# Performance work log

Measured on AMD Instinct MI355X. Metric: run time of the kernel, lower is better.

Reference implementation:

```python
import jax, jax.numpy as jnp
import numpy as np
from jax import lax

NFFT, WIN, HOP = 512, 320, 160
PAD = NFFT // 2
F = NFFT // 2 + 1  # 257

def _window():
    # torch.hann_window(320, periodic=True), center-padded to n_fft=512 (torch.stft convention)
    w = 0.5 - 0.5 * jnp.cos(2.0 * jnp.pi * jnp.arange(WIN, dtype=jnp.float32) / WIN)
    lp = (NFFT - WIN) // 2
    return jnp.pad(w, (lp, NFFT - WIN - lp))

def _stft(x):  # [N, L] -> [N, T, F] complex64 (center=True, reflect pad)
    xp = jnp.pad(x, ((0, 0), (PAD, PAD)), mode='reflect')
    T = 1 + (xp.shape[1] - NFFT) // HOP
    idx = jnp.arange(T)[:, None] * HOP + jnp.arange(NFFT)[None, :]
    frames = xp[:, idx] * _window()  # [N, T, NFFT]
    return jnp.fft.rfft(frames, axis=-1)

def _istft(spec, length):  # [N, T, F] complex -> [N, length]
    win = _window()
    frames = jnp.fft.irfft(spec, n=NFFT, axis=-1) * win  # [N, T, NFFT]
    N, T, _ = frames.shape
    total = (T - 1) * HOP + NFFT
    pos = (jnp.arange(T)[:, None] * HOP + jnp.arange(NFFT)[None, :]).reshape(-1)
    out = jnp.zeros((N, total), frames.dtype).at[:, pos].add(frames.reshape(N, -1))
    wsq = jnp.zeros((total,), win.dtype).at[pos].add(jnp.tile(win * win, T))
    out = out / jnp.maximum(wsq, 1e-11)[None, :]
    return out[:, PAD:PAD + length]

def _lstm(x, W_ih, W_hh, b_ih, b_hh):  # x [N, T, D] -> [N, T, H]
    N, T, _ = x.shape
    H = W_hh.shape[1]
    xW = x @ W_ih.T + (b_ih + b_hh)  # precompute input projections [N, T, 4H]
    def step(carry, xt):
        h, c = carry
        g = xt + h @ W_hh.T
        i, f, gg, o = jnp.split(g, 4, axis=-1)  # torch gate order i,f,g,o
        c = jax.nn.sigmoid(f) * c + jax.nn.sigmoid(i) * jnp.tanh(gg)
        h = jax.nn.sigmoid(o) * jnp.tanh(c)
        return (h, c), h
    h0 = jnp.zeros((N, H), x.dtype)
    _, hs = lax.scan(step, (h0, h0), jnp.swapaxes(xW, 0, 1))
    return jnp.swapaxes(hs, 0, 1)

def _forward(x, W_ih, W_hh, b_ih, b_hh, W1, b1, W2, b2):
    B, L, C = x.shape
    xm = jnp.transpose(x, (0, 2, 1)).reshape(B * C, L)
    spec = _stft(xm).reshape(B, C, -1, F)  # [B, C, T, F] == r_spec + 1j*i_spec
    T = spec.shape[2]
    feat = jnp.concatenate([spec.real, spec.imag], axis=-1).reshape(B * C, T, 2 * F)
    h = _lstm(feat, W_ih, W_hh, b_ih, b_hh)  # [B*C, T, 128]
    def masked(Wl, bl):
        m = h @ Wl.T + bl                      # [B*C, T, 514]
        rm, im = jnp.split(m, 2, axis=-1)
        mask = (rm + 1j * im).reshape(B, C, T, F)
        return mask * spec                      # complex mask multiply
    s_spec = masked(W1, b1)
    n_spec = masked(W2, b2)
    # per-frequency PSD matrices over time
    psd_s = jnp.einsum('bctf,betf->bfce', s_spec, jnp.conj(s_spec)) / T
    psd_n = jnp.einsum('bctf,betf->bfce', n_spec, jnp.conj(n_spec)) / T
    tr_n = jnp.einsum('bfcc->bf', psd_n).real
    eye = jnp.eye(C, dtype=psd_n.dtype)
    psd_n = psd_n + (1e-6 * tr_n / C + 1e-8)[..., None, None] * eye  # diagonal loading
    num = jnp.linalg.solve(psd_n, psd_s)                             # [B, F, C, C]
    ws = num / (jnp.einsum('bfcc->bf', num)[..., None, None] + 1e-8)
    w = ws[..., 0]                                                   # ref_channel = 0 -> [B, F, C]
    obs = jnp.transpose(spec, (0, 3, 1, 2))                          # [B, F, C, T]
    enh = jnp.einsum('bfc,bfct->bft', jnp.conj(w), obs)              # beamformed [B, F, T]
    return _istft(jnp.transpose(enh, (0, 2, 1)), L)                  # [B, L]

def setup_inputs() -> dict:
    key = jax.random.key(0)
    ks = jax.random.split(key, 8)
    D, H = 2 * F, 128
    s = 0.05
    return {
        'x': jax.random.normal(ks[0], (8, 96000, 8), jnp.float32),
        'W_ih': jax.random.normal(ks[1], (4 * H, D), jnp.float32) * s,
        'W_hh': jax.random.normal(ks[2], (4 * H, H), jnp.float32) * s,
        'b_ih': jnp.zeros((4 * H,), jnp.float32),
        'b_hh': jnp.zeros((4 * H,), jnp.float32),
        'W1': jax.random.normal(ks[3], (D, H), jnp.float32) * s,
        'b1': jnp.zeros((D,), jnp.float32),
        'W2': jax.random.normal(ks[4], (D, H), jnp.float32) * s,
        'b2': jnp.zeros((D,), jnp.float32),
    }

def reference(x, W_ih, W_hh, b_ih, b_hh, W1, b1, W2, b2):
    return _forward(x, W_ih, W_hh, b_ih, b_hh, W1, b1, W2, b2)
```

## Files before the change

kernel.cpp:

```cpp
#include <hip/hip_runtime.h>
#include <math.h>

#define NFFT  512
#define WINL  320
#define HOP   160
#define FPAD  256
#define NF    257
#define TT    601
#define LSEQ  96000
#define XPLEN 96512
#define NCH   8
#define NB    8
#define NSEQ  64
#define NROWS 38464
#define DD    514
#define HH    128
#define G4    512
#define KPAD  544
#define NCOMB 1026

typedef _Float16 h2v __attribute__((ext_vector_type(2)));
typedef short bf16x8 __attribute__((ext_vector_type(8)));
typedef float f32x4 __attribute__((ext_vector_type(4)));

__device__ __forceinline__ float winval(int k) {
  if (k < 96 || k >= 416) return 0.f;
  return 0.5f - 0.5f * cosf((float)(2.0 * M_PI / 320.0) * (float)(k - 96));
}

__device__ __forceinline__ void split_bf16(float v, unsigned short* h, unsigned short* l) {
  unsigned int hb = __float_as_uint(v) >> 16;
  float r = v - __uint_as_float(hb << 16);
  *h = (unsigned short)hb;
  *l = (unsigned short)(__float_as_uint(r) >> 16);
}

__global__ void k_wsq(float* __restrict__ wsq) {
  int p = blockIdx.x * 256 + threadIdx.x;
  if (p >= XPLEN) return;
  int t0 = (p <= 511) ? 0 : (p - 352) / 160;
  int t1 = p / 160; if (t1 > 600) t1 = 600;
  float s = 0.f;
  for (int t = t0; t <= t1; t++) { float w = winval(p - t * HOP); s += w * w; }
  wsq[p] = s;
}

__global__ void k_bff(float* __restrict__ BFf) {
  int idx = blockIdx.x * 256 + threadIdx.x;
  if (idx >= NFFT * DD) return;
  int k = idx / DD, d = idx - k * DD;
  float w = winval(k);
  int f = (d < NF) ? d : d - NF;
  int m = (k * f) & 511;
  float th = (float)(M_PI / 256.0) * (float)m;
  BFf[idx] = ((d < NF) ? cosf(th) : -sinf(th)) * w;
}

__global__ void k_wtsplit(const float* __restrict__ Wih, unsigned short* __restrict__ H,
                          unsigned short* __restrict__ L) {
  int idx = blockIdx.x * 256 + threadIdx.x;
  if (idx >= G4 * KPAD) return;
  int n = idx / KPAD, k = idx - n * KPAD;
  float v = (k < DD) ? Wih[n * DD + k] : 0.f;
  split_bf16(v, &H[idx], &L[idx]);
}

__global__ void k_bcomb(const float* __restrict__ BWf, unsigned short* __restrict__ H,
                        unsigned short* __restrict__ L) {
  int idx = blockIdx.x * 256 + threadIdx.x;
  if (idx >= 1152 * KPAD) return;
  int n = idx / KPAD, k = idx - n * KPAD;
  float v = 0.f;
  if (k < NFFT) {
    if (n < DD) {
      float w = winval(k);
      int f = (n < NF) ? n : n - NF;
      int m = (k * f) & 511;
      float th = (float)(M_PI / 256.0) * (float)m;
      v = ((n < NF) ? cosf(th) : -sinf(th)) * w;
    } else if (n < NCOMB) {
      v = BWf[k * G4 + (n - 514)];
    }
  }
  split_bf16(v, &H[idx], &L[idx]);
}

__global__ void k_bisplit(unsigned short* __restrict__ H, unsigned short* __restrict__ L) {
  int idx = blockIdx.x * 256 + threadIdx.x;
  if (idx >= NFFT * KPAD) return;
  int n = idx / KPAD, kk = idx - n * KPAD;
  float v = 0.f;
  if (kk < DD) {
    float w = winval(n);
    int f = (kk < NF) ? kk : kk - NF;
    int edge = (f == 0 || f == 256);
    float alpha = edge ? 1.f : 2.f;
    int m = (n * f) & 511;
    float th = (float)(M_PI / 256.0) * (float)m;
    float c;
    if (kk < NF) c = alpha * cosf(th);
    else         c = edge ? 0.f : -alpha * sinf(th);
    v = c * w * (1.f / 512.f);
  }
  split_bf16(v, &H[idx], &L[idx]);
}

__global__ void k_bsum(const float* __restrict__ bih, const float* __restrict__ bhh,
                       float* __restrict__ BSUM) {
  int idx = blockIdx.x * 256 + threadIdx.x;
  if (idx < G4) BSUM[idx] = bih[idx] + bhh[idx];
}

__global__ void k_wmsplit(const float* __restrict__ W1, const float* __restrict__ W2,
                          unsigned short* __restrict__ W1h, unsigned short* __restrict__ W1l,
                          unsigned short* __restrict__ W2h, unsigned short* __restrict__ W2l) {
  int idx = blockIdx.x * 256 + threadIdx.x;
  if (idx >= 2 * 640 * HH) return;
  int m = idx / (640 * HH);
  int rem = idx - m * 640 * HH;
  int np = rem / HH, k = rem - np * HH;
  int ri = np / 320, f = np - ri * 320;
  float v = 0.f;
  if (f < NF) {
    int fcol = (ri == 0) ? f : NF + f;
    v = (m == 0) ? W1[fcol * HH + k] : W2[fcol * HH + k];
  }
  unsigned short h, l;
  split_bf16(v, &h, &l);
  if (m == 0) { W1h[rem] = h; W1l[rem] = l; }
  else        { W2h[rem] = h; W2l[rem] = l; }
}

__global__ void k_wpack(const float* __restrict__ Whh, unsigned int* __restrict__ WhhP4) {
  int idx = blockIdx.x * 256 + threadIdx.x;
  if (idx >= G4 * 64) return;
  int j = idx >> 6, k2 = idx & 63;
  _Float16 lo = (_Float16)Whh[j * HH + 2 * k2];
  _Float16 hi = (_Float16)Whh[j * HH + 2 * k2 + 1];
  unsigned int u = ((unsigned int)__builtin_bit_cast(unsigned short, hi) << 16)
                 |  (unsigned int)__builtin_bit_cast(unsigned short, lo);
  WhhP4[(k2 >> 2) * (G4 * 4) + j * 4 + (k2 & 3)] = u;
}

__global__ void k_xp(const float* __restrict__ x, unsigned short* __restrict__ XPh,
                     unsigned short* __restrict__ XPl) {
  int idx = blockIdx.x * 256 + threadIdx.x;
  if (idx >= NSEQ * XPLEN) return;
  int n = idx / XPLEN, i = idx - n * XPLEN;
  int j = i - FPAD;
  if (j < 0) j = -j;
  else if (j >= LSEQ) j = 2 * LSEQ - 2 - j;
  int b = n >> 3, c = n & 7;
  float v = x[((long)b * LSEQ + j) * NCH + c];
  split_bf16(v, &XPh[idx], &XPl[idx]);
}

template <int GATHER>
__launch_bounds__(256)
__global__ void k_gemm3(const float* __restrict__ A,
                        const unsigned short* __restrict__ Bth,
                        const unsigned short* __restrict__ Btl,
                        const float* __restrict__ bias, float* __restrict__ C,
                        int M, int N, int K, int lda, int ldc) {
  __shared__ __align__(16) unsigned short sAh[128 * 40];
  __shared__ __align__(16) unsigned short sAl[128 * 40];
  __shared__ __align__(16) unsigned short sBh[128 * 40];
  __shared__ __align__(16) unsigned short sBl[128 * 40];
  const int tid = threadIdx.x;
  const int row0 = blockIdx.y * 128, col0 = blockIdx.x * 128;
  const int sar = tid >> 1, sak = (tid & 1) * 16;
  const int arow = row0 + sar;
  long abase = (long)arow * lda;
  const bool arok = (arow < M);
  const int lane = tid & 63, w = tid >> 6;
  const int wm = (w >> 1) * 64, wn = (w & 1) * 64;
  const int l15 = lane & 15, quad = lane >> 4;
  f32x4 acc[4][4] = {};
  unsigned int* aH = (unsigned int*)sAh;
  unsigned int* aL = (unsigned int*)sAl;
  uint4* bH = (uint4*)sBh;
  uint4* bL = (uint4*)sBl;
  for (int k0 = 0; k0 < K; k0 += 32) {
#pragma unroll
    for (int i = 0; i < 8; i++) {
      int kk = k0 + sak + 2 * i;
      float v0 = 0.f, v1 = 0.f;
      if (arok) {
        if (kk + 1 < K) { float2 t2 = *(const float2*)(A + abase + kk); v0 = t2.x; v1 = t2.y; }
        else if (kk < K) { v0 = A[abase + kk]; }
      }
      unsigned int h0 = __float_as_uint(v0) >> 16, h1 = __float_as_uint(v1) >> 16;
      float r0 = v0 - __uint_as_float(h0 << 16), r1 = v1 - __uint_as_float(h1 << 16);
      unsigned int l0 = __float_as_uint(r0) >> 16, l1 = __float_as_uint(r1) >> 16;
      aH[sar * 20 + (sak >> 1) + i] = h0 | (h1 << 16);
      aL[sar * 20 + (sak >> 1) + i] = l0 | (l1 << 16);
    }
#pragma unroll
    for (int h = 0; h < 2; h++) {
      int idx = tid + h * 256;
      int r = idx >> 2, c = idx & 3;
      long go = (long)(col0 + r) * KPAD + k0 + c * 8;
      bH[r * 5 + c] = *(const uint4*)(Bth + go);
      bL[r * 5 + c] = *(const uint4*)(Btl + go);
    }
    __syncthreads();
    bf16x8 ah[4], al[4], bh[4], bl[4];
#pragma unroll
    for (int i = 0; i < 4; i++) {
      int off = (wm + i * 16 + l15) * 40 + quad * 8;
      ah[i] = *(const bf16x8*)(sAh + off);
      al[i] = *(const bf16x8*)(sAl + off);
      int boff = (wn + i * 16 + l15) * 40 + quad * 8;
      bh[i] = *(const bf16x8*)(sBh + boff);
      bl[i] = *(const bf16x8*)(sBl + boff);
    }
#pragma unroll
    for (int i = 0; i < 4; i++)
#pragma unroll
      for (int j = 0; j < 4; j++) {
        acc[i][j] = __builtin_amdgcn_mfma_f32_16x16x32_bf16(al[i], bh[j], acc[i][j], 0, 0, 0);
        acc[i][j] = __builtin_amdgcn_mfma_f32_16x16x32_bf16(ah[i], bl[j], acc[i][j], 0, 0, 0);
        acc[i][j] = __builtin_amdgcn_mfma_f32_16x16x32_bf16(ah[i], bh[j], acc[i][j], 0, 0, 0);
      }
    __syncthreads();
  }
#pragma unroll
  for (int i = 0; i < 4; i++)
#pragma unroll
    for (int j = 0; j < 4; j++) {
      int cc = col0 + wn + j * 16 + l15;
      if (cc >= N) continue;
      float bv = bias ? bias[cc] : 0.f;
#pragma unroll
      for (int rg = 0; rg < 4; rg++) {
        int rr = row0 + wm + i * 16 + quad * 4 + rg;
        if (rr < M) C[(long)rr * ldc + cc] = acc[i][j][rg] + bv;
      }
    }
}

__launch_bounds__(256)
__global__ void k_gemm4(const unsigned short* __restrict__ Ah, const unsigned short* __restrict__ Al,
                        const unsigned short* __restrict__ Bh, const unsigned short* __restrict__ Bl,
                        const float* __restrict__ bsum, float* __restrict__ S,
                        float* __restrict__ XW) {
  __shared__ __align__(16) unsigned short sAh[128 * 40];
  __shared__ __align__(16) unsigned short sAl[128 * 40];
  __shared__ __align__(16) unsigned short sBh[128 * 40];
  __shared__ __align__(16) unsigned short sBl[128 * 40];
  const int tid = threadIdx.x;
  const int row0 = blockIdx.y * 128, col0 = blockIdx.x * 128;
  const int sr0 = tid >> 2, c4 = (tid & 3) * 8, cq = tid & 3;
  long ab0, ab1;
  { int rr = row0 + sr0;      int n = rr / TT, t = rr - n * TT; ab0 = (long)n * XPLEN + (long)t * HOP; }
  { int rr = row0 + sr0 + 64; int n = rr / TT, t = rr - n * TT; ab1 = (long)n * XPLEN + (long)t * HOP; }
  const int lane = tid & 63, w = tid >> 6;
  const int wm = (w >> 1) * 64, wn = (w & 1) * 64;
  const int l15 = lane & 15, quad = lane >> 4;
  f32x4 acc[4][4] = {};
  uint4* aH4 = (uint4*)sAh; uint4* aL4 = (uint4*)sAl;
  uint4* bH4 = (uint4*)sBh; uint4* bL4 = (uint4*)sBl;
  for (int k0 = 0; k0 < NFFT; k0 += 32) {
    aH4[sr0 * 5 + cq]        = *(const uint4*)(Ah + ab0 + k0 + c4);
    aL4[sr0 * 5 + cq]        = *(const uint4*)(Al + ab0 + k0 + c4);
    aH4[(sr0 + 64) * 5 + cq] = *(const uint4*)(Ah + ab1 + k0 + c4);
    aL4[(sr0 + 64) * 5 + cq] = *(const uint4*)(Al + ab1 + k0 + c4);
    {
      long go = (long)(col0 + sr0) * KPAD + k0 + c4;
      bH4[sr0 * 5 + cq] = *(const uint4*)(Bh + go);
      bL4[sr0 * 5 + cq] = *(const uint4*)(Bl + go);
      go = (long)(col0 + sr0 + 64) * KPAD + k0 + c4;
      bH4[(sr0 + 64) * 5 + cq] = *(const uint4*)(Bh + go);
      bL4[(sr0 + 64) * 5 + cq] = *(const uint4*)(Bl + go);
    }
    __syncthreads();
    bf16x8 ah[4], al[4], bh[4], bl[4];
#pragma unroll
    for (int i = 0; i < 4; i++) {
      int off = (wm + i * 16 + l15) * 40 + quad * 8;
      ah[i] = *(const bf16x8*)(sAh + off);
      al[i] = *(const bf16x8*)(sAl + off);
      int boff = (wn + i * 16 + l15) * 40 + quad * 8;
      bh[i] = *(const bf16x8*)(sBh + boff);
      bl[i] = *(const bf16x8*)(sBl + boff);
    }
#pragma unroll
    for (int i = 0; i < 4; i++)
#pragma unroll
      for (int j = 0; j < 4; j++) {
        acc[i][j] = __builtin_amdgcn_mfma_f32_16x16x32_bf16(al[i], bh[j], acc[i][j], 0, 0, 0);
        acc[i][j] = __builtin_amdgcn_mfma_f32_16x16x32_bf16(ah[i], bl[j], acc[i][j], 0, 0, 0);
        acc[i][j] = __builtin_amdgcn_mfma_f32_16x16x32_bf16(ah[i], bh[j], acc[i][j], 0, 0, 0);
      }
    __syncthreads();
  }
#pragma unroll
  for (int i = 0; i < 4; i++)
#pragma unroll
    for (int j = 0; j < 4; j++) {
      int cc = col0 + wn + j * 16 + l15;
      if (cc >= NCOMB) continue;
#pragma unroll
      for (int rg = 0; rg < 4; rg++) {
        int rr = row0 + wm + i * 16 + quad * 4 + rg;
        if (rr >= NROWS) continue;
        float v = acc[i][j][rg];
        if (cc < DD) S[(long)rr * DD + cc] = v;
        else         XW[(long)rr * G4 + (cc - 514)] = v + bsum[cc - 514];
      }
    }
}

__launch_bounds__(256)
__global__ void k_gemm5(const unsigned short* __restrict__ Ah, const unsigned short* __restrict__ Al,
                        const unsigned short* __restrict__ Bh, const unsigned short* __restrict__ Bl,
                        float* __restrict__ C, int M, int N, int ldc) {
  __shared__ __align__(16) unsigned short sAh[128 * 40];
  __shared__ __align__(16) unsigned short sAl[128 * 40];
  __shared__ __align__(16) unsigned short sBh[128 * 40];
  __shared__ __align__(16) unsigned short sBl[128 * 40];
  const int tid = threadIdx.x;
  const int row0 = blockIdx.y * 128, col0 = blockIdx.x * 128;
  const int sr0 = tid >> 2, c4 = (tid & 3) * 8, cq = tid & 3;
  const int lane = tid & 63, w = tid >> 6;
  const int wm = (w >> 1) * 64, wn = (w & 1) * 64;
  const int l15 = lane & 15, quad = lane >> 4;
  f32x4 acc[4][4] = {};
  uint4* aH4 = (uint4*)sAh; uint4* aL4 = (uint4*)sAl;
  uint4* bH4 = (uint4*)sBh; uint4* bL4 = (uint4*)sBl;
  for (int k0 = 0; k0 < KPAD; k0 += 32) {
    {
      long go = (long)(row0 + sr0) * KPAD + k0 + c4;
      aH4[sr0 * 5 + cq] = *(const uint4*)(Ah + go);
      aL4[sr0 * 5 + cq] = *(const uint4*)(Al + go);
      go = (long)(row0 + sr0 + 64) * KPAD + k0 + c4;
      aH4[(sr0 + 64) * 5 + cq] = *(const uint4*)(Ah + go);
      aL4[(sr0 + 64) * 5 + cq] = *(const uint4*)(Al + go);
    }
    {
      long go = (long)(col0 + sr0) * KPAD + k0 + c4;
      bH4[sr0 * 5 + cq] = *(const uint4*)(Bh + go);
      bL4[sr0 * 5 + cq] = *(const uint4*)(Bl + go);
      go = (long)(col0 + sr0 + 64) * KPAD + k0 + c4;
      bH4[(sr0 + 64) * 5 + cq] = *(const uint4*)(Bh + go);
      bL4[(sr0 + 64) * 5 + cq] = *(const uint4*)(Bl + go);
    }
    __syncthreads();
    bf16x8 ah[4], al[4], bh[4], bl[4];
#pragma unroll
    for (int i = 0; i < 4; i++) {
      int off = (wm + i * 16 + l15) * 40 + quad * 8;
      ah[i] = *(const bf16x8*)(sAh + off);
      al[i] = *(const bf16x8*)(sAl + off);
      int boff = (wn + i * 16 + l15) * 40 + quad * 8;
      bh[i] = *(const bf16x8*)(sBh + boff);
      bl[i] = *(const bf16x8*)(sBl + boff);
    }
#pragma unroll
    for (int i = 0; i < 4; i++)
#pragma unroll
      for (int j = 0; j < 4; j++) {
        acc[i][j] = __builtin_amdgcn_mfma_f32_16x16x32_bf16(al[i], bh[j], acc[i][j], 0, 0, 0);
        acc[i][j] = __builtin_amdgcn_mfma_f32_16x16x32_bf16(ah[i], bl[j], acc[i][j], 0, 0, 0);
        acc[i][j] = __builtin_amdgcn_mfma_f32_16x16x32_bf16(ah[i], bh[j], acc[i][j], 0, 0, 0);
      }
    __syncthreads();
  }
#pragma unroll
  for (int i = 0; i < 4; i++)
#pragma unroll
    for (int j = 0; j < 4; j++) {
      int cc = col0 + wn + j * 16 + l15;
      if (cc >= N) continue;
#pragma unroll
      for (int rg = 0; rg < 4; rg++) {
        int rr = row0 + wm + i * 16 + quad * 4 + rg;
        if (rr < M) C[(long)rr * ldc + cc] = acc[i][j][rg];
      }
    }
}

__device__ __forceinline__ float tanh_fast(float x) {
  float e = __expf(2.f * x);
  return 1.f - 2.f / (e + 1.f);
}

__launch_bounds__(512, 2)
__global__ void k_lstm(const float* __restrict__ XW, const unsigned int* __restrict__ WhhP4,
                       float* __restrict__ Hout) {
  __shared__ __align__(16) unsigned int hl2[64];
  __shared__ float gl[G4];
  const int j = threadIdx.x;
  const int n = blockIdx.x;
  const uint4* W4 = (const uint4*)WhhP4;
  unsigned int wp[64];
#pragma unroll
  for (int i4 = 0; i4 < 16; i4++) {
    uint4 v = W4[i4 * G4 + j];
    wp[4 * i4]     = v.x;
    wp[4 * i4 + 1] = v.y;
    wp[4 * i4 + 2] = v.z;
    wp[4 * i4 + 3] = v.w;
  }
  float cst = 0.f;
  if (j < 64) hl2[j] = 0u;
  const float* xwrow = XW + (long)n * TT * G4 + j;
  float xnext = xwrow[0];
  const uint4* h4 = (const uint4*)hl2;
  const bool isg = (j >= 2 * HH) && (j < 3 * HH);
  __syncthreads();
  for (int t = 0; t < TT; t++) {
    float xv = xnext;
    if (t + 1 < TT) xnext = xwrow[(long)(t + 1) * G4];
    float a0 = 0.f, a1 = 0.f, a2 = 0.f, a3 = 0.f;
#pragma unroll
    for (int k = 0; k < 16; k++) {
      uint4 hv4 = h4[k];
      a0 = __builtin_amdgcn_fdot2(__builtin_bit_cast(h2v, hv4.x), __builtin_bit_cast(h2v, wp[4 * k]),     a0, false);
      a1 = __builtin_amdgcn_fdot2(__builtin_bit_cast(h2v, hv4.y), __builtin_bit_cast(h2v, wp[4 * k + 1]), a1, false);
      a2 = __builtin_amdgcn_fdot2(__builtin_bit_cast(h2v, hv4.z), __builtin_bit_cast(h2v, wp[4 * k + 2]), a2, false);
      a3 = __builtin_amdgcn_fdot2(__builtin_bit_cast(h2v, hv4.w), __builtin_bit_cast(h2v, wp[4 * k + 3]), a3, false);
    }
    float a = ((a0 + a1) + (a2 + a3)) + xv;
    float nl;
    if (isg) nl = tanh_fast(a);
    else     nl = 1.f / (1.f + __expf(-a));
    gl[j] = nl;
    asm volatile("s_waitcnt lgkmcnt(0)" ::: "memory");
    __builtin_amdgcn_s_barrier();
    if (j < HH) {
      float ni = gl[j], nf = gl[HH + j], ng = gl[2 * HH + j], no = gl[3 * HH + j];
      cst = nf * cst + ni * ng;
      float hv = no * tanh_fast(cst);
      ((_Float16*)hl2)[j] = (_Float16)hv;
      Hout[((long)n * TT + t) * HH + j] = hv;
    }
    asm volatile("s_waitcnt lgkmcnt(0)" ::: "memory");
    __builtin_amdgcn_s_barrier();
  }
}

__launch_bounds__(256)
__global__ void k_maskms(const float* __restrict__ Hout,
                         const unsigned short* __restrict__ Wsh,
                         const unsigned short* __restrict__ Wsl,
                         const float* __restrict__ bias, const float* __restrict__ S,
                         float* __restrict__ MS) {
  __shared__ __align__(16) unsigned short sAh[64 * 40];
  __shared__ __align__(16) unsigned short sAl[64 * 40];
  __shared__ __align__(16) unsigned short sBh[64 * 40];
  __shared__ __align__(16) unsigned short sBl[64 * 40];
  __shared__ float Cs[64][68];
  __shared__ float SR[64][33];
  __shared__ float SI[64][33];
  const int tid = threadIdx.x;
  const int f0 = blockIdx.x * 32;
  const int row0 = blockIdx.y * 64;
  const int lane = tid & 63, w = tid >> 6;
  const int wm = w * 16;
  const int l15 = lane & 15, quad = lane >> 4;
  const int sar = tid >> 2;
  const int sak = (tid & 3) * 8;
  const int np = ((sar < 32) ? 0 : 320 - 32) + f0 + sar;
  unsigned int* aH = (unsigned int*)sAh;
  unsigned int* aL = (unsigned int*)sAl;
  f32x4 acc[4] = {};
  for (int k0 = 0; k0 < HH; k0 += 32) {
    {
      const float* ap = Hout + (long)(row0 + sar) * HH + k0 + sak;
      float4 v0 = *(const float4*)ap;
      float4 v1 = *(const float4*)(ap + 4);
      float vv[8] = {v0.x, v0.y, v0.z, v0.w, v1.x, v1.y, v1.z, v1.w};
#pragma unroll
      for (int i = 0; i < 4; i++) {
        unsigned int h0 = __float_as_uint(vv[2 * i]) >> 16, h1 = __float_as_uint(vv[2 * i + 1]) >> 16;
        float r0 = vv[2 * i] - __uint_as_float(h0 << 16), r1 = vv[2 * i + 1] - __uint_as_float(h1 << 16);
        unsigned int l0 = __float_as_uint(r0) >> 16, l1 = __float_as_uint(r1) >> 16;
        aH[sar * 20 + (sak >> 1) + i] = h0 | (h1 << 16);
        aL[sar * 20 + (sak >> 1) + i] = l0 | (l1 << 16);
      }
    }
    {
      long go = (long)np * HH + k0 + sak;
      *(uint4*)(sBh + sar * 40 + sak) = *(const uint4*)(Wsh + go);
      *(uint4*)(sBl + sar * 40 + sak) = *(const uint4*)(Wsl + go);
    }
    __syncthreads();
    bf16x8 ah = *(const bf16x8*)(sAh + (wm + l15) * 40 + quad * 8);
    bf16x8 al = *(const bf16x8*)(sAl + (wm + l15) * 40 + quad * 8);
#pragma unroll
    for (int ct = 0; ct < 4; ct++) {
      bf16x8 bh = *(const bf16x8*)(sBh + (ct * 16 + l15) * 40 + quad * 8);
      bf16x8 bl = *(const bf16x8*)(sBl + (ct * 16 + l15) * 40 + quad * 8);
      acc[ct] = __builtin_amdgcn_mfma_f32_16x16x32_bf16(al, bh, acc[ct], 0, 0, 0);
      acc[ct] = __builtin_amdgcn_mfma_f32_16x16x32_bf16(ah, bl, acc[ct], 0, 0, 0);
      acc[ct] = __builtin_amdgcn_mfma_f32_16x16x32_bf16(ah, bh, acc[ct], 0, 0, 0);
    }
    __syncthreads();
  }
#pragma unroll
  for (int ct = 0; ct < 4; ct++) {
    int col = ct * 16 + l15;
    int f = f0 + (col & 31);
    int fcol = (col < 32) ? f : NF + f;
    float bv = (f < NF) ? bias[fcol] : 0.f;
#pragma unroll
    for (int rg = 0; rg < 4; rg++) Cs[wm + quad * 4 + rg][col] = acc[ct][rg] + bv;
  }
  __syncthreads();
  {
    int fl = tid & 31, r8 = tid >> 5;
    int f = f0 + fl;
#pragma unroll
    for (int i = 0; i < 8; i++) {
      int rl = r8 * 8 + i;
      int rr = row0 + rl;
      float rm = Cs[rl][fl], im = Cs[rl][32 + fl];
      float sr = 0.f, si = 0.f;
      if (f < NF) { sr = S[(long)rr * DD + f]; si = S[(long)rr * DD + NF + f]; }
      SR[rl][fl] = rm * sr - im * si;
      SI[rl][fl] = rm * si + im * sr;
    }
  }
  __syncthreads();
  {
    int tl = tid & 63, fq = tid >> 6;
    int rr = row0 + tl;
    int n = rr / TT, t = rr - n * TT;
    int b = n >> 3, c = n & 7;
#pragma unroll
    for (int i = 0; i < 8; i++) {
      int fl = fq * 8 + i;
      int f = f0 + fl;
      if (f < NF) {
        long addr = ((((long)b * NF + f) * 8 + c) * (long)TT + t) * 2;
        *(float2*)&MS[addr] = make_float2(SR[tl][fl], SI[tl][fl]);
      }
    }
  }
}

__launch_bounds__(256)
__global__ void k_psd(const float* __restrict__ MS, float* __restrict__ PSD) {
  __shared__ float buf[9616];
  __shared__ float part[64][8];
  const int tid = threadIdx.x;
  const long base = (long)blockIdx.x * 9616;
  for (int i = tid; i < 9616; i += 256) buf[i] = MS[base + i];
  __syncthreads();
  int p = tid & 63, q = tid >> 6;
  int c = p >> 3, e = p & 7;
  const float2* xc = (const float2*)&buf[c * 1202];
  const float2* xe = (const float2*)&buf[e * 1202];
  int t0 = q * 150, t1 = (q == 3) ? TT : t0 + 150;
  float ar = 0.f, ai = 0.f;
  for (int t = t0; t < t1; t++) {
    float2 m = xc[t];
    float2 v = xe[t];
    ar += m.x * v.x + m.y * v.y;
    ai += m.y * v.x - m.x * v.y;
  }
  part[p][q * 2] = ar; part[p][q * 2 + 1] = ai;
  __syncthreads();
  if (tid < 64) {
    float sr = part[tid][0] + part[tid][2] + part[tid][4] + part[tid][6];
    float si = part[tid][1] + part[tid][3] + part[tid][5] + part[tid][7];
    PSD[((long)blockIdx.x * 64 + tid) * 2]     = sr * (1.f / 601.f);
    PSD[((long)blockIdx.x * 64 + tid) * 2 + 1] = si * (1.f / 601.f);
  }
}

__launch_bounds__(64)
__global__ void k_solve(const float* __restrict__ PS, const float* __restrict__ PN,
                        float* __restrict__ WV) {
  int idx = blockIdx.x * 64 + threadIdx.x;
  if (idx >= NB * NF) return;
  float Ar[8][8], Ai[8][8], Br[8][8], Bi[8][8];
  const float* pn = PN + (long)idx * 128;
  const float* ps = PS + (long)idx * 128;
  for (int i = 0; i < 8; i++)
    for (int j = 0; j < 8; j++) {
      Ar[i][j] = pn[(i * 8 + j) * 2]; Ai[i][j] = pn[(i * 8 + j) * 2 + 1];
      Br[i][j] = ps[(i * 8 + j) * 2]; Bi[i][j] = ps[(i * 8 + j) * 2 + 1];
    }
  float tr = 0.f;
  for (int i = 0; i < 8; i++) tr += Ar[i][i];
  float load = 1e-6f * tr / 8.f + 1e-8f;
  for (int i = 0; i < 8; i++) Ar[i][i] += load;
  for (int k = 0; k < 8; k++) {
    int piv = k; float mx = Ar[k][k] * Ar[k][k] + Ai[k][k] * Ai[k][k];
    for (int i = k + 1; i < 8; i++) {
      float m2 = Ar[i][k] * Ar[i][k] + Ai[i][k] * Ai[i][k];
      if (m2 > mx) { mx = m2; piv = i; }
    }
    if (piv != k) {
      for (int j = 0; j < 8; j++) {
        float t0;
        t0 = Ar[k][j]; Ar[k][j] = Ar[piv][j]; Ar[piv][j] = t0;
        t0 = Ai[k][j]; Ai[k][j] = Ai[piv][j]; Ai[piv][j] = t0;
        t0 = Br[k][j]; Br[k][j] = Br[piv][j]; Br[piv][j] = t0;
        t0 = Bi[k][j]; Bi[k][j] = Bi[piv][j]; Bi[piv][j] = t0;
      }
    }
    float dr = Ar[k][k], di = Ai[k][k];
    float inv = 1.f / (dr * dr + di * di);
    float irr = dr * inv, iii = -di * inv;
    for (int j = 0; j < 8; j++) {
      float xr = Ar[k][j], xi = Ai[k][j];
      Ar[k][j] = xr * irr - xi * iii; Ai[k][j] = xr * iii + xi * irr;
      xr = Br[k][j]; xi = Bi[k][j];
      Br[k][j] = xr * irr - xi * iii; Bi[k][j] = xr * iii + xi * irr;
    }
    for (int i = 0; i < 8; i++) {
      if (i == k) continue;
      float fr = Ar[i][k], fi = Ai[i][k];
      for (int j = 0; j < 8; j++) {
        float kr = Ar[k][j], ki = Ai[k][j];
        Ar[i][j] -= fr * kr - fi * ki;
        Ai[i][j] -= fr * ki + fi * kr;
        kr = Br[k][j]; ki = Bi[k][j];
        Br[i][j] -= fr * kr - fi * ki;
        Bi[i][j] -= fr * ki + fi * kr;
      }
    }
  }
  float trr = 1e-8f, tri = 0.f;
  for (int i = 0; i < 8; i++) { trr += Br[i][i]; tri += Bi[i][i]; }
  float inv = 1.f / (trr * trr + tri * tri);
  for (int c = 0; c < 8; c++) {
    float xr = Br[c][0], xi = Bi[c][0];
    WV[((long)idx * 8 + c) * 2]     = (xr * trr + xi * tri) * inv;
    WV[((long)idx * 8 + c) * 2 + 1] = (xi * trr - xr * tri) * inv;
  }
}

__launch_bounds__(320)
__global__ void k_beam(const float* __restrict__ S, const float* __restrict__ WV,
                       unsigned short* __restrict__ ENHh, unsigned short* __restrict__ ENHl) {
  __shared__ float WL[NF * 16];
  int bb = blockIdx.x / TT, t = blockIdx.x - bb * TT;
  for (int i = threadIdx.x; i < NF * 16; i += 320) WL[i] = WV[(long)bb * NF * 16 + i];
  __syncthreads();
  int f = threadIdx.x;
  long base = ((long)bb * TT + t) * KPAD;
  if (f < NF) {
    float er = 0.f, ei = 0.f;
#pragma unroll
    for (int c = 0; c < 8; c++) {
      float wr = WL[(f * 8 + c) * 2], wi = WL[(f * 8 + c) * 2 + 1];
      const float* srow = S + (((long)(bb * 8 + c) * TT) + t) * DD;
      float sr = srow[f], si = srow[NF + f];
      er += wr * sr + wi * si;
      ei += wr * si - wi * sr;
    }
    split_bf16(er, &ENHh[base + f], &ENHl[base + f]);
    split_bf16(ei, &ENHh[base + NF + f], &ENHl[base + NF + f]);
  }
  int z = threadIdx.x - 288;
  if (z >= 0 && z < 30) { ENHh[base + DD + z] = 0; ENHl[base + DD + z] = 0; }
}

__global__ void k_ola(const float* __restrict__ IFR, const float* __restrict__ WSQ,
                      float* __restrict__ out) {
  int idx = blockIdx.x * 256 + threadIdx.x;
  if (idx >= NB * LSEQ) return;
  int b = idx / LSEQ, l = idx - b * LSEQ;
  int p = l + FPAD;
  int t0 = (p <= 511) ? 0 : (p - 352) / 160;
  int t1 = p / 160; if (t1 > 600) t1 = 600;
  float s = 0.f;
  for (int t = t0; t <= t1; t++) s += IFR[((long)b * TT + t) * NFFT + (p - t * HOP)];
  out[idx] = s / fmaxf(WSQ[p], 1e-11f);
}

extern "C" void kernel_launch(void* const* d_in, const int* in_sizes, int n_in,
                              void* d_out, int out_size, void* d_ws, size_t ws_size,
                              hipStream_t stream) {
  (void)in_sizes; (void)n_in; (void)out_size; (void)ws_size;
  const float* x   = (const float*)d_in[0];
  const float* Wih = (const float*)d_in[1];
  const float* Whh = (const float*)d_in[2];
  const float* bih = (const float*)d_in[3];
  const float* bhh = (const float*)d_in[4];
  const float* W1  = (const float*)d_in[5];
  const float* b1  = (const float*)d_in[6];
  const float* W2  = (const float*)d_in[7];
  const float* b2  = (const float*)d_in[8];
  float* ws = (float*)d_ws;

  unsigned short* XPh = (unsigned short*)(ws + 0);
  unsigned short* XPl = (unsigned short*)(ws + 3088384);
  float* S     = ws + 6176768;
  float* XWM   = ws + 25951264;
  float* HOUT  = ws + 45725760;
  float* PSD_S = ws + 50650048;
  float* PSD_N = ws + 50913216;
  float* WV    = ws + 51176384;
  float* BSUM  = ws + 51209280;
  float* WSQ   = ws + 51209792;
  unsigned short* W1sh = (unsigned short*)(ws + 51306304);
  unsigned short* W1sl = (unsigned short*)(ws + 51347264);
  unsigned short* W2sh = (unsigned short*)(ws + 51388224);
  unsigned short* W2sl = (unsigned short*)(ws + 51429184);
  unsigned short* WTth = (unsigned short*)(ws + 51470144);
  unsigned short* WTtl = (unsigned short*)(ws + 51609408);
  unsigned short* BIth = (unsigned short*)(ws + 51748672);
  unsigned short* BItl = (unsigned short*)(ws + 51887936);
  float* MS    = XWM;
  float* IFR   = ws + 0;
  unsigned int* WhhP4 = (unsigned int*)(XWM + 19693568);
  float* BFf = HOUT;
  float* BWf = HOUT + 263168;
  unsigned short* BCh = (unsigned short*)(HOUT + 525312);
  unsigned short* BCl = (unsigned short*)(HOUT + 838656);
  unsigned short* ENHh = (unsigned short*)HOUT;
  unsigned short* ENHl = (unsigned short*)(HOUT + 1307776);

  k_wsq<<<(XPLEN + 255) / 256, 256, 0, stream>>>(WSQ);
  k_bff<<<(NFFT * DD + 255) / 256, 256, 0, stream>>>(BFf);
  k_wtsplit<<<(G4 * KPAD + 255) / 256, 256, 0, stream>>>(Wih, WTth, WTtl);
  k_bisplit<<<(NFFT * KPAD + 255) / 256, 256, 0, stream>>>(BIth, BItl);
  k_bsum<<<2, 256, 0, stream>>>(bih, bhh, BSUM);
  k_wmsplit<<<(2 * 640 * HH + 255) / 256, 256, 0, stream>>>(W1, W2, W1sh, W1sl, W2sh, W2sl);
  k_wpack<<<(G4 * 64 + 255) / 256, 256, 0, stream>>>(Whh, WhhP4);
  k_xp<<<(NSEQ * XPLEN + 255) / 256, 256, 0, stream>>>(x, XPh, XPl);

  {
    dim3 g(4, 4);
    k_gemm3<0><<<g, 256, 0, stream>>>(BFf, WTth, WTtl, nullptr, BWf, 512, 512, DD, DD, G4);
  }
  k_bcomb<<<(1152 * KPAD + 255) / 256, 256, 0, stream>>>(BWf, BCh, BCl);

  {
    dim3 g(9, 301);
    k_gemm4<<<g, 256, 0, stream>>>(XPh, XPl, BCh, BCl, BSUM, S, XWM);
  }

  k_lstm<<<64, 512, 0, stream>>>(XWM, WhhP4, HOUT);

  dim3 gm(9, 601);
  k_maskms<<<gm, 256, 0, stream>>>(HOUT, W1sh, W1sl, b1, S, MS);
  k_psd<<<NB * NF, 256, 0, stream>>>(MS, PSD_S);
  k_maskms<<<gm, 256, 0, stream>>>(HOUT, W2sh, W2sl, b2, S, MS);
  k_psd<<<NB * NF, 256, 0, stream>>>(MS, PSD_N);

  k_solve<<<(NB * NF + 63) / 64, 64, 0, stream>>>(PSD_S, PSD_N, WV);
  k_beam<<<NB * TT, 320, 0, stream>>>(S, WV, ENHh, ENHl);

  {
    dim3 g(4, 38);
    k_gemm5<<<g, 256, 0, stream>>>(ENHh, ENHl, BIth, BItl, IFR, NB * TT, NFFT, NFFT);
  }

  k_ola<<<(NB * LSEQ + 255) / 256, 256, 0, stream>>>(IFR, WSQ, (float*)d_out);
}
```

Baseline: 1.160 ms.

## Remap LSTM gate rows so gates combine via wave shuffles, one barrier per step

Each wave's lanes are reassigned so that the four gates (i,f,g,o) for a hidden unit sit in four quads of the same wave. The gates are then exchanged with xor shuffles instead of a shared-memory round trip. The hidden state is double-buffered in LDS, which removes one of the two block barriers per timestep in the sequential recurrence. Every lane now computes all gate nonlinearities redundantly, adding some ALU work to save LDS traffic and synchronisation.

```diff
diff --git a/kernel.cpp b/kernel.cpp
--- a/kernel.cpp
+++ b/kernel.cpp
@@ -388,30 +388,35 @@
 __launch_bounds__(512, 2)
 __global__ void k_lstm(const float* __restrict__ XW, const unsigned int* __restrict__ WhhP4,
                        float* __restrict__ Hout) {
-  __shared__ __align__(16) unsigned int hl2[64];
-  __shared__ float gl[G4];
+  __shared__ __align__(16) unsigned int hl2[2][64];
   const int j = threadIdx.x;
   const int n = blockIdx.x;
+  const int w = j >> 6, lane = j & 63;
+  const int l15 = lane & 15, quad = lane >> 4;
+  const int row = quad * 128 + 16 * w + l15;
   const uint4* W4 = (const uint4*)WhhP4;
   unsigned int wp[64];
 #pragma unroll
   for (int i4 = 0; i4 < 16; i4++) {
-    uint4 v = W4[i4 * G4 + j];
+    uint4 v = W4[i4 * G4 + row];
     wp[4 * i4]     = v.x;
     wp[4 * i4 + 1] = v.y;
     wp[4 * i4 + 2] = v.z;
     wp[4 * i4 + 3] = v.w;
   }
   float cst = 0.f;
-  if (j < 64) hl2[j] = 0u;
-  const float* xwrow = XW + (long)n * TT * G4 + j;
+  if (j < 64) hl2[0][j] = 0u;
+  const float* xwrow = XW + (long)n * TT * G4 + row;
   float xnext = xwrow[0];
-  const uint4* h4 = (const uint4*)hl2;
-  const bool isg = (j >= 2 * HH) && (j < 3 * HH);
+  const bool q0 = (quad & 1) != 0;
+  const bool q1 = (quad >> 1) != 0;
+  float* hop = Hout + (long)n * TT * HH + 16 * w + l15;
   __syncthreads();
   for (int t = 0; t < TT; t++) {
+    const int cur = t & 1;
     float xv = xnext;
     if (t + 1 < TT) xnext = xwrow[(long)(t + 1) * G4];
+    const uint4* h4 = (const uint4*)hl2[cur];
     float a0 = 0.f, a1 = 0.f, a2 = 0.f, a3 = 0.f;
 #pragma unroll
     for (int k = 0; k < 16; k++) {
@@ -422,18 +427,20 @@
       a3 = __builtin_amdgcn_fdot2(__builtin_bit_cast(h2v, hv4.w), __builtin_bit_cast(h2v, wp[4 * k + 3]), a3, false);
     }
     float a = ((a0 + a1) + (a2 + a3)) + xv;
-    float nl;
-    if (isg) nl = tanh_fast(a);
-    else     nl = 1.f / (1.f + __expf(-a));
-    gl[j] = nl;
-    asm volatile("s_waitcnt lgkmcnt(0)" ::: "memory");
-    __builtin_amdgcn_s_barrier();
-    if (j < HH) {
-      float ni = gl[j], nf = gl[HH + j], ng = gl[2 * HH + j], no = gl[3 * HH + j];
-      cst = nf * cst + ni * ng;
-      float hv = no * tanh_fast(cst);
-      ((_Float16*)hl2)[j] = (_Float16)hv;
-      Hout[((long)n * TT + t) * HH + j] = hv;
+    float b = __shfl_xor(a, 16);
+    float c = __shfl_xor(a, 32);
+    float d = __shfl_xor(b, 32);
+    float t0 = q0 ? b : a, t1 = q0 ? a : b, t2 = q0 ? d : c, t3 = q0 ? c : d;
+    float gi = q1 ? t2 : t0, gf = q1 ? t3 : t1, gg = q1 ? t0 : t2, go = q1 ? t1 : t3;
+    float si = 1.f / (1.f + __expf(-gi));
+    float sf = 1.f / (1.f + __expf(-gf));
+    float tg = tanh_fast(gg);
+    float so = 1.f / (1.f + __expf(-go));
+    cst = sf * cst + si * tg;
+    float hv = so * tanh_fast(cst);
+    if (quad == 0) {
+      ((_Float16*)hl2[cur ^ 1])[16 * w + l15] = (_Float16)hv;
+      hop[(long)t * HH] = hv;
     }
     asm volatile("s_waitcnt lgkmcnt(0)" ::: "memory");
     __builtin_amdgcn_s_barrier();
```

Result: slower. 1.247 ms (+7.5%).
